# Optimization experiments

Measured on AMD Instinct MI355X. Metric: run time of the kernel, lower is better.

The kernel has to match this reference:

```python
import jax, jax.numpy as jnp
import numpy as np
from jax import lax

EPS = 1e-5

def _ln(x, g, b):
    m = x.mean(-1, keepdims=True)
    v = x.var(-1, keepdims=True)
    return (x - m) * lax.rsqrt(v + EPS) * g + b

def _conv(x, w, b=None, groups=1, pad=0):
    y = lax.conv_general_dilated(x, w, (1, 1), [(pad, pad), (pad, pad)],
                                 feature_group_count=groups,
                                 dimension_numbers=('NCHW', 'OIHW', 'NCHW'))
    return y if b is None else y + b[None, :, None, None]

def _pscan(A, X):
    # linear recurrence h_t = A_t * h_{t-1} + X_t via associative scan over axis 1
    def comb(c1, c2):
        a1, x1 = c1
        a2, x2 = c2
        return a1 * a2, a2 * x1 + x2
    return lax.associative_scan(comb, (A, X), axis=1)[1]

def setup_inputs():
    B, T, D, H, W, K, E = 2, 24, 32, 64, 64, 3, 2
    key = jax.random.key(0)
    ks = jax.random.split(key, 30)
    r = lambda i, shp, s=1.0: jax.random.normal(ks[i], shp, jnp.float32) * s
    return dict(
        x_re=r(0, (B, T, D, H, W)), x_im=r(1, (B, T, D, H, W)),
        h_re=r(2, (B * H * W, 1, D)), h_im=r(3, (B * H * W, 1, D)),
        flux_re=r(4, (B, D), 0.5), flux_im=r(5, (B, D), 0.5),
        dt_seq=jax.random.uniform(ks[6], (B, T), jnp.float32, 0.05, 0.15),
        ln_s_g=jnp.ones((2 * D,)), ln_s_b=jnp.zeros((2 * D,)),
        conv_w=r(7, (2 * D, 2 * D, K, K), 0.05), conv_b=jnp.zeros((2 * D,)),
        ln_t_g=jnp.ones((2 * D,)), ln_t_b=jnp.zeros((2 * D,)),
        W_re=jnp.eye(D, dtype=jnp.float32) + r(8, (D, D), 0.1), W_im=r(9, (D, D), 0.1),
        lam_flux=r(10, (D,), 0.5), bf_re=r(11, (D,), 0.5), bf_im=r(12, (D,), 0.5),
        c_re=r(13, (D,), 0.5), c_im=r(14, (D,), 0.5),
        g_w=r(15, (D,), 0.5), g_b=jnp.zeros((D,)),
        a_decay=r(16, (D,), 0.5), b_freq=r(17, (D,), 0.5),
        ffn_w1=r(18, (2 * D, 2 * D * E), 0.05), ffn_b1=jnp.zeros((2 * D * E,)),
        ffn_w2=r(19, (2 * D * E, 2 * D), 0.05), ffn_b2=jnp.zeros((2 * D,)),
        sg_w1=r(20, (D, 2 * D, 1, 1), 0.05), sg_b1=jnp.zeros((D,)),
        sg_dw=r(21, (D, 1, 3, 3), 0.05),
        sg_w2=r(22, (D, D, 1, 1), 0.05), sg_b2=jnp.zeros((D,)),
    )

def reference(x_re, x_im, h_re, h_im, flux_re, flux_im, dt_seq,
              ln_s_g, ln_s_b, conv_w, conv_b, ln_t_g, ln_t_b,
              W_re, W_im, lam_flux, bf_re, bf_im, c_re, c_im, g_w, g_b,
              a_decay, b_freq, ffn_w1, ffn_b1, ffn_w2, ffn_b2,
              sg_w1, sg_b1, sg_dw, sg_w2, sg_b2):
    x = x_re + 1j * x_im                                  # [B,T,D,H,W] complex64
    B, T, D, H, W = x.shape
    K = conv_w.shape[-1]
    # ---- spatial (Clifford-style) conv with residual ----
    xf = x.reshape(B * T, D, H, W)
    xr = jnp.concatenate([xf.real, xf.imag], axis=1)      # [BT,2D,H,W]
    xn = _ln(xr.transpose(0, 2, 3, 1), ln_s_g, ln_s_b).transpose(0, 3, 1, 2)
    xs = _conv(xn, conv_w, conv_b, pad=K // 2)
    xf = xf + (xs[:, :D] + 1j * xs[:, D:])
    x = xf.reshape(B, T, D, H, W)
    # ---- eigen-basis encode ----
    Wb = W_re + 1j * W_im
    Wb_inv = jnp.linalg.inv(Wb)
    x_eig = jnp.einsum('bthwd,de->bthwe', x.transpose(0, 1, 3, 4, 2), Wb)  # [B,T,H,W,D]
    x_mean = x_eig.mean(axis=(2, 3))                      # [B,T,D]
    # ---- global flux scan over time ----
    dt = dt_seq[:, :, None]                               # [B,T,1]
    A_flux = jnp.exp(-jax.nn.softplus(lam_flux) * dt).astype(x_eig.dtype)  # [B,T,D]
    X_flux = (bf_re + 1j * bf_im) * x_mean * dt
    flux_seq = _pscan(A_flux, X_flux)
    flux_seq = flux_seq + (flux_re + 1j * flux_im)[:, None, :] * jnp.cumprod(A_flux, axis=1)
    source_seq = flux_seq * (c_re + 1j * c_im)            # [B,T,D] complex
    gate_seq = jax.nn.sigmoid(flux_seq.real * g_w + g_b)  # [B,T,D] real
    flux_out = flux_seq[:, -1]
    # ---- spatial gate modulation, batched over B*T (no python loop over T) ----
    xc = jnp.concatenate([x_eig.real, x_eig.imag], axis=-1)        # [B,T,H,W,2D]
    sf = xc.reshape(B * T, H, W, 2 * D).transpose(0, 3, 1, 2)
    g = jax.nn.silu(_conv(sf, sg_w1, sg_b1))
    g = _conv(g, sg_dw, None, groups=D, pad=1)
    g = jax.nn.sigmoid(_conv(g, sg_w2, sg_b2))                     # [BT,D,H,W]
    sp_gate = g.transpose(0, 2, 3, 1).reshape(B, T, H, W, D)
    gate_comb = gate_seq[:, :, None, None, :] * sp_gate            # [B,T,H,W,D]
    src = source_seq[:, :, None, None, :]
    forcing = x_eig * gate_comb + src * (1.0 - gate_comb)
    # ---- transition operators (ZOH discretization) ----
    lam = -jax.nn.softplus(a_decay) + 1j * b_freq                  # [D]
    op_decay = jnp.exp(lam * dt)                                   # [B,T,D] complex
    op_forcing = (op_decay - 1.0) / lam
    u_t = forcing * op_forcing[:, :, None, None, :]
    h_prev = (h_re + 1j * h_im).reshape(B, H, W, D)
    u_t = u_t.at[:, 0].add(h_prev * op_decay[:, 0][:, None, None, :])
    # ---- per-pixel temporal pscan ----
    A_full = jnp.broadcast_to(op_decay[:, :, None, None, :], u_t.shape)
    u_out = _pscan(A_full, u_t)                                    # [B,T,H,W,D]
    h_out = u_out[:, -1].reshape(B * H * W, 1, D)
    # ---- decode + temporal LN/FFN residual ----
    dec = jnp.einsum('bthwe,ed->bthwd', u_out, Wb_inv).transpose(0, 1, 4, 2, 3)
    df = dec.reshape(B * T, D, H, W)
    dr = jnp.concatenate([df.real, df.imag], axis=1).transpose(0, 2, 3, 1)  # [BT,H,W,2D]
    dn = _ln(dr, ln_t_g, ln_t_b)
    hid = jax.nn.silu(dn @ ffn_w1 + ffn_b1)
    out2 = hid @ ffn_w2 + ffn_b2
    delta = (out2[..., :D] + 1j * out2[..., D:]).transpose(0, 3, 1, 2)
    xo = (df + delta).reshape(B, T, D, H, W)
    z = x + xo
    out_main = jnp.stack([z.real, z.imag], axis=0)
    out_h = jnp.stack([h_out.real, h_out.imag], axis=0)
    out_flux = jnp.stack([flux_out.real, flux_out.imag], axis=0)
    return out_main, out_h, out_flux
```

## Files before the change

kernel.cpp:

```cpp
#include <hip/hip_runtime.h>
#include <math.h>

#define BB 2
#define TT 24
#define DD 32
#define HWp 4096
#define NN (BB*TT)
#define PIX (NN*HWp)
#define C2 (2*DD)

#define MAIN_RE 0
#define MAIN_IM (NN*DD*HWp)
#define HOUT_RE (2*NN*DD*HWp)
#define HOUT_IM (HOUT_RE + BB*HWp*DD)
#define FLUX_RE (HOUT_RE + 2*BB*HWp*DD)
#define FLUX_IM (FLUX_RE + BB*DD)

#define WS_XN   0
#define WS_XU   (WS_XN + PIX*32)
#define WS_XE   (WS_XU + PIX*32)
#define WS_G1   (WS_XE + PIX*C2)
#define WS_G2   (WS_G1 + PIX*DD)
#define WS_WINV (WS_G2 + PIX*DD)
#define WS_SUMS (WS_WINV + 2048)
#define WS_GATE (WS_SUMS + 3072)
#define WS_SRCR (WS_GATE + 1536)
#define WS_SRCI (WS_SRCR + 1536)
#define WS_ODR  (WS_SRCI + 1536)
#define WS_ODI  (WS_ODR + 1536)
#define WS_OFR  (WS_ODI + 1536)
#define WS_OFI  (WS_OFR + 1536)
#define WS_WPK  (WS_OFI + 1536)
#define WS_PART (WS_WPK + 18432)
#define WS_WE   (WS_PART + 49152)
#define WS_SG   (WS_WE + 2048)
#define WS_WIB  (WS_SG + 1024)

typedef __attribute__((ext_vector_type(8))) short bf16x8;
typedef __attribute__((ext_vector_type(4))) float f32x4;
union FU { unsigned u[4]; bf16x8 f; };
union FU4 { uint4 v; unsigned u[4]; bf16x8 f; };

__device__ __forceinline__ float sigmoidf_(float x) { return 1.f / (1.f + expf(-x)); }
__device__ __forceinline__ float softplusf_(float x) { return log1pf(expf(x)); }
__device__ __forceinline__ unsigned short f2bf(float f) {
  unsigned u = __float_as_uint(f);
  return (unsigned short)((u + 0x7FFFu + ((u >> 16) & 1u)) >> 16);
}
__device__ __forceinline__ unsigned pk2(float lo, float hi) {
  return (unsigned)f2bf(lo) | ((unsigned)f2bf(hi) << 16);
}
__device__ __forceinline__ float bf2f(unsigned short u) {
  return __uint_as_float((unsigned)u << 16);
}

__global__ void __launch_bounds__(256) k_prep(
    const float* __restrict__ xre, const float* __restrict__ xim,
    const float* __restrict__ g, const float* __restrict__ b,
    const float* __restrict__ Wre, const float* __restrict__ Wim,
    const float* __restrict__ conv_w, const float* __restrict__ sgw1,
    float* __restrict__ ws) {
  int bid = blockIdx.x;
  int tid = threadIdx.x;

  if (bid < 768) {
    int gid = bid * 256 + tid;
    int n = gid >> 12, p = gid & 4095;
    float v[64];
    float s = 0.f;
#pragma unroll
    for (int c = 0; c < 32; ++c) { v[c] = xre[(n * 32 + c) * 4096 + p]; s += v[c]; }
#pragma unroll
    for (int c = 0; c < 32; ++c) { v[32 + c] = xim[(n * 32 + c) * 4096 + p]; s += v[32 + c]; }
    float m = s * (1.f / 64.f);
    float vs = 0.f;
#pragma unroll
    for (int c = 0; c < 64; ++c) { float d = v[c] - m; vs += d * d; }
    float rs = rsqrtf(vs * (1.f / 64.f) + 1e-5f);
#pragma unroll
    for (int c = 0; c < 64; ++c) v[c] = (v[c] - m) * rs * g[c] + b[c];
    uint4* dst = (uint4*)ws + gid * 8;
#pragma unroll
    for (int q = 0; q < 8; ++q) {
      uint4 u;
      u.x = pk2(v[q * 8 + 0], v[q * 8 + 1]);
      u.y = pk2(v[q * 8 + 2], v[q * 8 + 3]);
      u.z = pk2(v[q * 8 + 4], v[q * 8 + 5]);
      u.w = pk2(v[q * 8 + 6], v[q * 8 + 7]);
      dst[q] = u;
    }
    return;
  }

  if (bid <= 783) {
    int slice = bid - 768;
    unsigned short* wpk = (unsigned short*)(ws + WS_WPK);
#pragma unroll
    for (int i = 0; i < 9; ++i) {
      int idx = slice * 2304 + i * 256 + tid;
      int tap = idx >> 12;
      int rem = idx & 4095;
      int oc = rem >> 6, ci = rem & 63;
      wpk[idx] = f2bf(conv_w[(oc * 64 + ci) * 9 + tap]);
    }
    return;
  }

  {
    int t = (bid - 784) * 256 + tid;
    unsigned* we = (unsigned*)(ws + WS_WE);
    unsigned* sg = (unsigned*)(ws + WS_SG);
    {
      int oc = t >> 5, kp = t & 31;
      sg[t] = pk2(sgw1[oc * 64 + 2 * kp], sgw1[oc * 64 + 2 * kp + 1]);
    }
#pragma unroll
    for (int h2 = 0; h2 < 2; ++h2) {
      int idx = t + h2 * 1024;
      int j = idx >> 5, kp = idx & 31;
      float v[2];
#pragma unroll
      for (int h = 0; h < 2; ++h) {
        int k = 2 * kp + h;
        float x;
        if (j < 32) x = (k < 32) ? Wre[k * 32 + j] : -Wim[(k - 32) * 32 + j];
        else        x = (k < 32) ? Wim[k * 32 + (j - 32)] : Wre[(k - 32) * 32 + (j - 32)];
        v[h] = x;
      }
      we[idx] = pk2(v[0], v[1]);
    }
  }
}

__global__ void __launch_bounds__(256) k_conv(
    const unsigned* __restrict__ xnb_u, const unsigned short* __restrict__ wpk,
    const float* __restrict__ bconv,
    const float* __restrict__ xre, const float* __restrict__ xim,
    unsigned* __restrict__ xub,
    const float* __restrict__ Wre, const float* __restrict__ Wim,
    unsigned* __restrict__ wib) {
  __shared__ unsigned xls[8448];
  __shared__ int piv_s;
  __shared__ float prs[2];
  int bid = blockIdx.x;
  int tid = threadIdx.x;

  if (bid == 0) {
    float* Mre = (float*)xls;
    float* Mim = (float*)xls + 2048;
    float* fre = (float*)xls + 4096;
    float* fim = (float*)xls + 4128;
    for (int idx = tid; idx < 2048; idx += 256) {
      int i = idx >> 6, j = idx & 63;
      if (j < 32) { Mre[idx] = Wre[i * 32 + j]; Mim[idx] = Wim[i * 32 + j]; }
      else        { Mre[idx] = (j - 32 == i) ? 1.f : 0.f; Mim[idx] = 0.f; }
    }
    __syncthreads();
    for (int k = 0; k < 32; ++k) {
      if (tid < 32) {
        int r = tid;
        float re = Mre[r * 64 + k], im = Mim[r * 64 + k];
        float mm = (r >= k) ? (fabsf(re) + fabsf(im)) : -1.f;
        int best = r;
#pragma unroll
        for (int off = 16; off > 0; off >>= 1) {
          float m2 = __shfl_xor(mm, off);
          int b2 = __shfl_xor(best, off);
          if (m2 > mm || (m2 == mm && b2 < best)) { mm = m2; best = b2; }
        }
        float pvr = __shfl(re, best);
        float pvi = __shfl(im, best);
        if (tid == 0) {
          float dd = pvr * pvr + pvi * pvi;
          piv_s = best;
          prs[0] = pvr / dd;
          prs[1] = -pvi / dd;
        }
      }
      __syncthreads();
      int pv = piv_s;
      float pr = prs[0], pi = prs[1];
      if (tid < 64) {
        int l = tid;
        float kr = Mre[k * 64 + l], ki = Mim[k * 64 + l];
        float vr = Mre[pv * 64 + l], vi = Mim[pv * 64 + l];
        Mre[pv * 64 + l] = kr; Mim[pv * 64 + l] = ki;
        Mre[k * 64 + l] = vr * pr - vi * pi;
        Mim[k * 64 + l] = vr * pi + vi * pr;
        if (l == k) { fre[pv] = kr; fim[pv] = ki; }
        if (l < 32 && l != pv && l != k) {
          fre[l] = Mre[l * 64 + k];
          fim[l] = Mim[l * 64 + k];
        }
      }
      __syncthreads();
      for (int idx = tid; idx < 2048; idx += 256) {
        int i = idx >> 6, j = idx & 63;
        if (i != k) {
          float fr = fre[i], fi2 = fim[i];
          float ar = Mre[k * 64 + j], ai = Mim[k * 64 + j];
          Mre[idx] -= fr * ar - fi2 * ai;
          Mim[idx] -= fr * ai + fi2 * ar;
        }
      }
      __syncthreads();
    }
    for (int idx = tid; idx < 2048; idx += 256) {
      int j = idx >> 5, kp = idx & 31;
      float v[2];
#pragma unroll
      for (int h = 0; h < 2; ++h) {
        int kk = 2 * kp + h;
        float x;
        if (j < 32) x = (kk < 32) ? Mre[kk * 64 + 32 + j] : -Mim[(kk - 32) * 64 + 32 + j];
        else        x = (kk < 32) ? Mim[kk * 64 + 32 + (j - 32)] : Mre[(kk - 32) * 64 + 32 + (j - 32)];
        v[h] = x;
      }
      wib[idx] = pk2(v[0], v[1]);
    }
    return;
  }

  int cb = bid - 1;
  int n = cb >> 4;
  int y0 = (cb & 15) * 4;
  int wv = tid >> 6, l = tid & 63;
  int l15 = l & 15, l4 = l >> 4;

  const uint4* xnb4 = (const uint4*)xnb_u;

  f32x4 acc[4][4];
#pragma unroll
  for (int Nt = 0; Nt < 4; ++Nt) {
    float bb = bconv[Nt * 16 + l15];
#pragma unroll
    for (int mt = 0; mt < 4; ++mt) acc[mt][Nt] = (f32x4){bb, bb, bb, bb};
  }

  const uint4* wq = (const uint4*)wpk;
#pragma unroll
  for (int h = 0; h < 2; ++h) {
    if (h) __syncthreads();
    for (int idx = tid; idx < 396; idx += 256) {
      int r = idx / 66, c = idx - r * 66;
      int y = y0 - 1 + r, x = c - 1;
      bool valid = ((unsigned)y < 64u) & ((unsigned)x < 64u);
      int pg = n * 4096 + y * 64 + x;
      uint4 z; z.x = z.y = z.z = z.w = 0u;
#pragma unroll
      for (int q = 0; q < 4; ++q) {
        uint4 v = valid ? xnb4[pg * 8 + h * 4 + q] : z;
        *(uint4*)&xls[idx * 20 + q * 4] = v;
      }
    }
    __syncthreads();

#pragma unroll
    for (int tap = 0; tap < 9; ++tap) {
      int ky = tap / 3, kx = tap - ky * 3;
      int rowbase = (wv + ky) * 66 + kx + l15;
      FU4 B[4];
#pragma unroll
      for (int Nt = 0; Nt < 4; ++Nt)
        B[Nt].v = wq[tap * 512 + (Nt * 16 + l15) * 8 + h * 4 + l4];
#pragma unroll
      for (int mt = 0; mt < 4; ++mt) {
        FU4 A;
        A.v = *(const uint4*)&xls[(rowbase + mt * 16) * 20 + l4 * 4];
#pragma unroll
        for (int Nt = 0; Nt < 4; ++Nt)
          acc[mt][Nt] = __builtin_amdgcn_mfma_f32_16x16x32_bf16(A.f, B[Nt].f, acc[mt][Nt], 0, 0, 0);
      }
    }
  }
  __syncthreads();

  unsigned short (*xsb)[66] = (unsigned short(*)[66])xls;
#pragma unroll
  for (int Nt = 0; Nt < 4; ++Nt) {
    int oc = Nt * 16 + l15;
    int d = oc & 31;
    const float* resid = (oc < 32) ? xre : xim;
    const float* rsd = resid + (n * 32 + d) * 4096;
#pragma unroll
    for (int mt = 0; mt < 4; ++mt) {
      int lp0 = wv * 64 + mt * 16 + l4 * 4;
      int pixbase = y0 * 64 + lp0;
#pragma unroll
      for (int r = 0; r < 4; ++r)
        xsb[lp0 + r][oc] = f2bf(rsd[pixbase + r] + acc[mt][Nt][r]);
    }
  }
  __syncthreads();

  int pixG0 = n * 4096 + y0 * 64;
#pragma unroll
  for (int i = 0; i < 8; ++i) {
    int idx = tid + 256 * i;
    int lp = idx >> 3, q4 = idx & 7;
    uint4 v;
    v.x = xls[lp * 33 + q4 * 4 + 0];
    v.y = xls[lp * 33 + q4 * 4 + 1];
    v.z = xls[lp * 33 + q4 * 4 + 2];
    v.w = xls[lp * 33 + q4 * 4 + 3];
    ((uint4*)xub)[(pixG0 + lp) * 8 + q4] = v;
  }
}

__global__ void __launch_bounds__(256) k_xeig(
    const unsigned* __restrict__ xub, const unsigned* __restrict__ weP,
    const unsigned* __restrict__ sgP, unsigned short* __restrict__ xeb,
    unsigned short* __restrict__ g1b, const float* __restrict__ sgb1,
    float* __restrict__ part) {
  __shared__ unsigned WeT[64][35];
  __shared__ unsigned SgT[32][35];
  __shared__ unsigned xp[64][35];
  __shared__ float xef[64][67];

  int tid = threadIdx.x;
  int gbase = blockIdx.x * 256;
  int l = tid & 63, wv = tid >> 6;
  int l15 = l & 15, l4 = l >> 4;
  int p64 = l, q = wv;
  const uint4* xub4 = (const uint4*)xub;

  {
#pragma unroll
    for (int i = 0; i < 8; ++i) {
      int idx = tid + i * 256;
      WeT[idx >> 5][idx & 31] = weP[idx];
    }
#pragma unroll
    for (int i = 0; i < 4; ++i) {
      int idx = tid + i * 256;
      SgT[idx >> 5][idx & 31] = sgP[idx];
    }
  }
  float ssum[16];
#pragma unroll
  for (int i = 0; i < 16; ++i) ssum[i] = 0.f;
  __syncthreads();

  for (int ph = 0; ph < 4; ++ph) {
    int gg = gbase + ph * 64 + p64;
    int arow = wv * 16 + l15;
    int pixG = gbase + ph * 64 + arow;

    FU4 a0, a1;
    a0.v = xub4[pixG * 8 + l4];
    a1.v = xub4[pixG * 8 + 4 + l4];
#pragma unroll
    for (int Nt = 0; Nt < 4; ++Nt) {
      f32x4 acc = (f32x4){0.f, 0.f, 0.f, 0.f};
      FU b0f, b1f;
      int brow = Nt * 16 + l15;
#pragma unroll
      for (int jj = 0; jj < 4; ++jj) {
        b0f.u[jj] = WeT[brow][l4 * 4 + jj];
        b1f.u[jj] = WeT[brow][16 + l4 * 4 + jj];
      }
      acc = __builtin_amdgcn_mfma_f32_16x16x32_bf16(a0.f, b0f.f, acc, 0, 0, 0);
      acc = __builtin_amdgcn_mfma_f32_16x16x32_bf16(a1.f, b1f.f, acc, 0, 0, 0);
#pragma unroll
      for (int r = 0; r < 4; ++r)
        xef[wv * 16 + l4 * 4 + r][Nt * 16 + l15] = acc[r];
    }
    __syncthreads();

    float xo[16];
#pragma unroll
    for (int i = 0; i < 16; ++i) {
      xo[i] = xef[p64][q * 16 + i];
      ssum[i] += xo[i];
      xeb[(q * 16 + i) * PIX + gg] = f2bf(xo[i]);
    }
#pragma unroll
    for (int ii = 0; ii < 8; ++ii)
      xp[p64][q * 8 + ii] = pk2(xo[2 * ii], xo[2 * ii + 1]);
    __syncthreads();

    FU c0, c1;
#pragma unroll
    for (int jj = 0; jj < 4; ++jj) {
      c0.u[jj] = xp[arow][l4 * 4 + jj];
      c1.u[jj] = xp[arow][16 + l4 * 4 + jj];
    }
#pragma unroll
    for (int Nt = 0; Nt < 2; ++Nt) {
      float bb = sgb1[Nt * 16 + l15];
      f32x4 acc = (f32x4){bb, bb, bb, bb};
      FU b0f, b1f;
      int brow = Nt * 16 + l15;
#pragma unroll
      for (int jj = 0; jj < 4; ++jj) {
        b0f.u[jj] = SgT[brow][l4 * 4 + jj];
        b1f.u[jj] = SgT[brow][16 + l4 * 4 + jj];
      }
      acc = __builtin_amdgcn_mfma_f32_16x16x32_bf16(c0.f, b0f.f, acc, 0, 0, 0);
      acc = __builtin_amdgcn_mfma_f32_16x16x32_bf16(c1.f, b1f.f, acc, 0, 0, 0);
#pragma unroll
      for (int r = 0; r < 4; ++r) {
        float v = acc[r];
        xef[wv * 16 + l4 * 4 + r][Nt * 16 + l15] = v * sigmoidf_(v);
      }
    }
    __syncthreads();

#pragma unroll
    for (int i = 0; i < 8; ++i)
      g1b[(q * 8 + i) * PIX + gg] = f2bf(xef[p64][q * 8 + i]);
    __syncthreads();
  }

#pragma unroll
  for (int i = 0; i < 16; ++i) {
    float v = ssum[i];
    v += __shfl_xor(v, 1);
    v += __shfl_xor(v, 2);
    v += __shfl_xor(v, 4);
    v += __shfl_xor(v, 8);
    v += __shfl_xor(v, 16);
    v += __shfl_xor(v, 32);
    if (l == 0) part[blockIdx.x * 64 + q * 16 + i] = v;
  }
}

__global__ void k_flux(float* __restrict__ ws, float* __restrict__ out,
                       const float* __restrict__ dt_seq,
                       const float* __restrict__ flux_re, const float* __restrict__ flux_im,
                       const float* __restrict__ lam_flux,
                       const float* __restrict__ bf_re, const float* __restrict__ bf_im,
                       const float* __restrict__ c_re, const float* __restrict__ c_im,
                       const float* __restrict__ g_w, const float* __restrict__ g_b,
                       const float* __restrict__ a_decay, const float* __restrict__ b_freq) {
  int tid = threadIdx.x;
  if (tid >= 64) return;
  int b = tid >> 5, e = tid & 31;
  float sp_lf = softplusf_(lam_flux[e]);
  float lr = -softplusf_(a_decay[e]);
  float li = b_freq[e];
  float den = lr * lr + li * li;
  float bfr = bf_re[e], bfi = bf_im[e];
  float cr = c_re[e], ci = c_im[e];
  float fr = flux_re[b * 32 + e], fi = flux_im[b * 32 + e];
  const float* part = ws + WS_PART;
  for (int t = 0; t < 24; ++t) {
    int n = b * 24 + t;
    float dt = dt_seq[n];
    float A = expf(-sp_lf * dt);
    float xmr = 0.f, xmi = 0.f;
#pragma unroll
    for (int j = 0; j < 16; ++j) {
      xmr += part[(n * 16 + j) * 64 + e];
      xmi += part[(n * 16 + j) * 64 + 32 + e];
    }
    xmr *= (1.f / 4096.f);
    xmi *= (1.f / 4096.f);
    float Xr = (bfr * xmr - bfi * xmi) * dt;
    float Xi = (bfr * xmi + bfi * xmr) * dt;
    fr = A * fr + Xr;
    fi = A * fi + Xi;
    ws[WS_GATE + n * 32 + e] = sigmoidf_(fr * g_w[e] + g_b[e]);
    ws[WS_SRCR + n * 32 + e] = fr * cr - fi * ci;
    ws[WS_SRCI + n * 32 + e] = fr * ci + fi * cr;
    float er = expf(lr * dt);
    float odr = er * cosf(li * dt);
    float odi = er * sinf(li * dt);
    ws[WS_ODR + n * 32 + e] = odr;
    ws[WS_ODI + n * 32 + e] = odi;
    float nr = odr - 1.f, ni = odi;
    ws[WS_OFR + n * 32 + e] = (nr * lr + ni * li) / den;
    ws[WS_OFI + n * 32 + e] = (ni * lr - nr * li) / den;
  }
  out[FLUX_RE + b * 32 + e] = fr;
  out[FLUX_IM + b * 32 + e] = fi;
}

__global__ void __launch_bounds__(256) k_gate(
    const unsigned short* __restrict__ g1b, unsigned short* __restrict__ spgb,
    const float* __restrict__ dw, const float* __restrict__ w2,
    const float* __restrict__ b2) {
  __shared__ float g2s[128][33];
  int tid = threadIdx.x;
  int l = tid & 63;
  int wv = tid >> 6;
  int r = wv >> 1, h = wv & 1;
  int pixbase = blockIdx.x * 128;
  int n = pixbase >> 12;
  int y = ((pixbase & 4095) >> 6) + r;
  int g = pixbase + r * 64 + l;
  int rp = r * 64 + l;

#pragma unroll
  for (int c = 0; c < 16; ++c) {
    int oc = h * 16 + c;
    const unsigned short* src = g1b + oc * PIX + n * 4096;
    const float* w = dw + oc * 9;
    float r0 = (y > 0)  ? bf2f(src[(y - 1) * 64 + l]) : 0.f;
    float r1 = bf2f(src[y * 64 + l]);
    float r2 = (y < 63) ? bf2f(src[(y + 1) * 64 + l]) : 0.f;
    float l0 = __shfl_up(r0, 1), t0 = __shfl_down(r0, 1);
    float l1 = __shfl_up(r1, 1), t1 = __shfl_down(r1, 1);
    float l2 = __shfl_up(r2, 1), t2 = __shfl_down(r2, 1);
    if (l == 0)  { l0 = 0.f; l1 = 0.f; l2 = 0.f; }
    if (l == 63) { t0 = 0.f; t1 = 0.f; t2 = 0.f; }
    float acc = 0.f;
    acc = fmaf(l0, w[0], acc); acc = fmaf(r0, w[1], acc); acc = fmaf(t0, w[2], acc);
    acc = fmaf(l1, w[3], acc); acc = fmaf(r1, w[4], acc); acc = fmaf(t1, w[5], acc);
    acc = fmaf(l2, w[6], acc); acc = fmaf(r2, w[7], acc); acc = fmaf(t2, w[8], acc);
    g2s[rp][oc] = acc;
  }
  __syncthreads();
  float g2a[32];
#pragma unroll
  for (int c = 0; c < 32; ++c) g2a[c] = g2s[rp][c];

#pragma unroll
  for (int c = 0; c < 16; ++c) {
    int e = h * 16 + c;
    float acc = b2[e];
#pragma unroll
    for (int k = 0; k < 32; ++k)
      acc = fmaf(g2a[k], w2[e * 32 + k], acc);
    spgb[e * PIX + g] = f2bf(sigmoidf_(acc));
  }
}

__global__ void __launch_bounds__(256) k_scan(
    unsigned short* __restrict__ ub, const unsigned short* __restrict__ spgb,
    const float* __restrict__ gate, const float* __restrict__ srcr,
    const float* __restrict__ srci, const float* __restrict__ ofr_p,
    const float* __restrict__ ofi_p, const float* __restrict__ odr_p,
    const float* __restrict__ odi_p,
    const float* __restrict__ hre, const float* __restrict__ him,
    float* __restrict__ out) {
  int p = blockIdx.x * 256 + threadIdx.x;
  int e = blockIdx.y;
  int b = blockIdx.z;
  float ur = 0.f, ui = 0.f;
  for (int t = 0; t < 24; ++t) {
    int n = b * 24 + t;
    int ie = n * 32 + e;
    int idx  = e * PIX + n * 4096 + p;
    int idxi = (32 + e) * PIX + n * 4096 + p;
    float gc = gate[ie] * bf2f(spgb[idx]);
    float xr = bf2f(ub[idx]), xi = bf2f(ub[idxi]);
    float om = 1.f - gc;
    float fr2 = xr * gc + srcr[ie] * om;
    float fi2 = xi * gc + srci[ie] * om;
    float ofr = ofr_p[ie], ofi = ofi_p[ie];
    float utr = fr2 * ofr - fi2 * ofi;
    float uti = fr2 * ofi + fi2 * ofr;
    if (t == 0) {
      int hb = (b * 4096 + p) * 32 + e;
      float hr = hre[hb], hi = him[hb];
      float odr0 = odr_p[ie], odi0 = odi_p[ie];
      utr += hr * odr0 - hi * odi0;
      uti += hr * odi0 + hi * odr0;
    }
    float ar = odr_p[ie], ai = odi_p[ie];
    float nr = ar * ur - ai * ui + utr;
    float ni = ar * ui + ai * ur + uti;
    ur = nr; ui = ni;
    ub[idx] = f2bf(ur);
    ub[idxi] = f2bf(ui);
  }
  out[HOUT_RE + (b * 4096 + p) * 32 + e] = ur;
  out[HOUT_IM + (b * 4096 + p) * 32 + e] = ui;
}

__global__ void __launch_bounds__(256) k_final(
    const unsigned short* __restrict__ ub, const unsigned* __restrict__ xub,
    float* __restrict__ out, const unsigned* __restrict__ wibP,
    const float* __restrict__ lg, const float* __restrict__ lb,
    const float* __restrict__ w1, const float* __restrict__ b1,
    const float* __restrict__ w2, const float* __restrict__ b2) {
  __shared__ unsigned wiT[64][35];
  __shared__ unsigned w1T[128][35];
  __shared__ unsigned w2T[64][67];
  __shared__ unsigned dnp[64][35];
  __shared__ unsigned ho[64][67];
  __shared__ float ps1[64][5];
  __shared__ float ps2[64][5];

  int tid = threadIdx.x;
  int gbase = blockIdx.x * 256;
  int l = tid & 63, wv = tid >> 6;
  int l15 = l & 15, l4 = l >> 4;
  int p64 = l, q = wv;
  const uint4* xub4 = (const uint4*)xub;

  {
#pragma unroll
    for (int i = 0; i < 8; ++i) {
      int idx = tid + i * 256;
      wiT[idx >> 5][idx & 31] = wibP[idx];
    }
    int hid = tid & 127, half = tid >> 7;
#pragma unroll
    for (int i = 0; i < 16; ++i) {
      int cp = half * 16 + i;
      w1T[hid][cp] = pk2(w1[(2 * cp) * 128 + hid], w1[(2 * cp + 1) * 128 + hid]);
    }
#pragma unroll
    for (int i = 0; i < 16; ++i) {
      int hp = wv * 16 + i;
      w2T[l][hp] = pk2(w2[(2 * hp) * 64 + l], w2[(2 * hp + 1) * 64 + l]);
    }
  }
  float bb1v[8], bb2v[4];
#pragma unroll
  for (int Hn = 0; Hn < 8; ++Hn) bb1v[Hn] = b1[Hn * 16 + l15];
#pragma unroll
  for (int On = 0; On < 4; ++On) bb2v[On] = b2[On * 16 + l15];

  unsigned uvp[8];
  FU4 xa, xb;
  {
    int gg = gbase + p64;
#pragma unroll
    for (int ii = 0; ii < 8; ++ii) {
      int c0 = q * 16 + 2 * ii;
      unsigned lo = ub[c0 * PIX + gg];
      unsigned hi = ub[(c0 + 1) * PIX + gg];
      uvp[ii] = lo | (hi << 16);
    }
    xa.v = xub4[gg * 8 + q * 2];
    xb.v = xub4[gg * 8 + q * 2 + 1];
  }
  __syncthreads();

  for (int ph = 0; ph < 4; ++ph) {
    int gg = gbase + ph * 64 + p64;
    int arow = wv * 16 + l15;

#pragma unroll
    for (int ii = 0; ii < 8; ++ii)
      dnp[p64][q * 8 + ii] = uvp[ii];
    if (ph < 3) {
      int gg2 = gg + 64;
#pragma unroll
      for (int ii = 0; ii < 8; ++ii) {
        int c0 = q * 16 + 2 * ii;
        unsigned lo = ub[c0 * PIX + gg2];
        unsigned hi = ub[(c0 + 1) * PIX + gg2];
        uvp[ii] = lo | (hi << 16);
      }
    }
    __syncthreads();

    {
      FU a0, a1;
#pragma unroll
      for (int jj = 0; jj < 4; ++jj) {
        a0.u[jj] = dnp[arow][l4 * 4 + jj];
        a1.u[jj] = dnp[arow][16 + l4 * 4 + jj];
      }
      float (*decf)[67] = (float(*)[67])ho;
#pragma unroll
      for (int Nt = 0; Nt < 4; ++Nt) {
        f32x4 acc = (f32x4){0.f, 0.f, 0.f, 0.f};
        FU b0f, b1f;
        int brow = Nt * 16 + l15;
#pragma unroll
        for (int jj = 0; jj < 4; ++jj) {
          b0f.u[jj] = wiT[brow][l4 * 4 + jj];
          b1f.u[jj] = wiT[brow][16 + l4 * 4 + jj];
        }
        acc = __builtin_amdgcn_mfma_f32_16x16x32_bf16(a0.f, b0f.f, acc, 0, 0, 0);
        acc = __builtin_amdgcn_mfma_f32_16x16x32_bf16(a1.f, b1f.f, acc, 0, 0, 0);
#pragma unroll
        for (int r = 0; r < 4; ++r)
          decf[wv * 16 + l4 * 4 + r][Nt * 16 + l15] = acc[r];
      }
    }
    __syncthreads();

    float dv[16];
    float s1 = 0.f, s2 = 0.f;
    {
      float (*decf)[67] = (float(*)[67])ho;
#pragma unroll
      for (int i = 0; i < 16; ++i) {
        dv[i] = decf[p64][q * 16 + i];
        s1 += dv[i];
        s2 += dv[i] * dv[i];
      }
    }
    ps1[p64][q] = s1;
    ps2[p64][q] = s2;
    __syncthreads();
    float m  = (ps1[p64][0] + ps1[p64][1] + ps1[p64][2] + ps1[p64][3]) * (1.f / 64.f);
    float e2 = (ps2[p64][0] + ps2[p64][1] + ps2[p64][2] + ps2[p64][3]) * (1.f / 64.f);
    float rs = rsqrtf(e2 - m * m + 1e-5f);
#pragma unroll
    for (int ii = 0; ii < 8; ++ii) {
      int c0 = q * 16 + 2 * ii;
      float a = (dv[2 * ii]     - m) * rs * lg[c0]     + lb[c0];
      float bvl = (dv[2 * ii + 1] - m) * rs * lg[c0 + 1] + lb[c0 + 1];
      dnp[p64][q * 8 + ii] = pk2(a, bvl);
    }
    __syncthreads();

    FU a0, a1;
#pragma unroll
    for (int jj = 0; jj < 4; ++jj) {
      a0.u[jj] = dnp[arow][l4 * 4 + jj];
      a1.u[jj] = dnp[arow][16 + l4 * 4 + jj];
    }
    f32x4 acc[8];
#pragma unroll
    for (int Hn = 0; Hn < 8; ++Hn) {
      float bb = bb1v[Hn];
      acc[Hn] = (f32x4){bb, bb, bb, bb};
      FU b0f, b1f;
      int brow = Hn * 16 + l15;
#pragma unroll
      for (int jj = 0; jj < 4; ++jj) {
        b0f.u[jj] = w1T[brow][l4 * 4 + jj];
        b1f.u[jj] = w1T[brow][16 + l4 * 4 + jj];
      }
      acc[Hn] = __builtin_amdgcn_mfma_f32_16x16x32_bf16(a0.f, b0f.f, acc[Hn], 0, 0, 0);
      acc[Hn] = __builtin_amdgcn_mfma_f32_16x16x32_bf16(a1.f, b1f.f, acc[Hn], 0, 0, 0);
    }
    unsigned short (*hidb)[134] = (unsigned short(*)[134])ho;
#pragma unroll
    for (int Hn = 0; Hn < 8; ++Hn) {
#pragma unroll
      for (int r = 0; r < 4; ++r) {
        float v = acc[Hn][r];
        v = v * sigmoidf_(v);
        hidb[wv * 16 + l4 * 4 + r][Hn * 16 + l15] = f2bf(v);
      }
    }
    __syncthreads();

    FU a2[4];
#pragma unroll
    for (int kk = 0; kk < 4; ++kk)
#pragma unroll
      for (int jj = 0; jj < 4; ++jj)
        a2[kk].u[jj] = ((unsigned(*)[67])ho)[arow][kk * 16 + l4 * 4 + jj];
    f32x4 acc2[4];
#pragma unroll
    for (int On = 0; On < 4; ++On) {
      float bb = bb2v[On];
      acc2[On] = (f32x4){bb, bb, bb, bb};
#pragma unroll
      for (int kk = 0; kk < 4; ++kk) {
        FU b2f;
#pragma unroll
        for (int jj = 0; jj < 4; ++jj)
          b2f.u[jj] = w2T[On * 16 + l15][kk * 16 + l4 * 4 + jj];
        acc2[On] = __builtin_amdgcn_mfma_f32_16x16x32_bf16(a2[kk].f, b2f.f, acc2[On], 0, 0, 0);
      }
    }
    float (*o2f)[67] = (float(*)[67])ho;
#pragma unroll
    for (int On = 0; On < 4; ++On)
#pragma unroll
      for (int r = 0; r < 4; ++r)
        o2f[wv * 16 + l4 * 4 + r][On * 16 + l15] = acc2[On][r];
    __syncthreads();

    {
      int nn = gg >> 12, pim = gg & 4095;
#pragma unroll
      for (int ii = 0; ii < 8; ++ii) {
        unsigned w = (ii < 4) ? xa.u[ii] : xb.u[ii - 4];
        float x0 = __uint_as_float(w << 16);
        float x1 = __uint_as_float(w & 0xFFFF0000u);
        int c0 = q * 16 + 2 * ii;
#pragma unroll
        for (int h = 0; h < 2; ++h) {
          int c = c0 + h;
          float xv = (h == 0) ? x0 : x1;
          float val = xv + o2f[p64][c] + dv[2 * ii + h];
          int d = c & 31;
          long off = ((c < 32) ? (long)MAIN_RE : (long)MAIN_IM) + (long)(nn * 32 + d) * 4096 + pim;
          out[off] = val;
        }
      }
      if (ph < 3) {
        int gg2 = gg + 64;
        xa.v = xub4[gg2 * 8 + q * 2];
        xb.v = xub4[gg2 * 8 + q * 2 + 1];
      }
    }
    __syncthreads();
  }
}

extern "C" void kernel_launch(void* const* d_in, const int* in_sizes, int n_in,
                              void* d_out, int out_size, void* d_ws, size_t ws_size,
                              hipStream_t stream) {
  (void)in_sizes; (void)n_in; (void)out_size; (void)ws_size;
  const float* xre      = (const float*)d_in[0];
  const float* xim      = (const float*)d_in[1];
  const float* hre      = (const float*)d_in[2];
  const float* him      = (const float*)d_in[3];
  const float* flux_re  = (const float*)d_in[4];
  const float* flux_im  = (const float*)d_in[5];
  const float* dt_seq   = (const float*)d_in[6];
  const float* ln_s_g   = (const float*)d_in[7];
  const float* ln_s_b   = (const float*)d_in[8];
  const float* conv_w   = (const float*)d_in[9];
  const float* conv_b   = (const float*)d_in[10];
  const float* ln_t_g   = (const float*)d_in[11];
  const float* ln_t_b   = (const float*)d_in[12];
  const float* W_re     = (const float*)d_in[13];
  const float* W_im     = (const float*)d_in[14];
  const float* lam_flux = (const float*)d_in[15];
  const float* bf_re    = (const float*)d_in[16];
  const float* bf_im    = (const float*)d_in[17];
  const float* c_re     = (const float*)d_in[18];
  const float* c_im     = (const float*)d_in[19];
  const float* g_w      = (const float*)d_in[20];
  const float* g_b      = (const float*)d_in[21];
  const float* a_decay  = (const float*)d_in[22];
  const float* b_freq   = (const float*)d_in[23];
  const float* ffn_w1   = (const float*)d_in[24];
  const float* ffn_b1   = (const float*)d_in[25];
  const float* ffn_w2   = (const float*)d_in[26];
  const float* ffn_b2   = (const float*)d_in[27];
  const float* sg_w1    = (const float*)d_in[28];
  const float* sg_b1    = (const float*)d_in[29];
  const float* sg_dw    = (const float*)d_in[30];
  const float* sg_w2    = (const float*)d_in[31];
  const float* sg_b2    = (const float*)d_in[32];
  float* out = (float*)d_out;
  float* ws  = (float*)d_ws;

  unsigned* xub = (unsigned*)(ws + WS_XU);
  unsigned short* xeb = (unsigned short*)(ws + WS_XE);
  unsigned short* g1b = (unsigned short*)(ws + WS_G1);
  unsigned short* spgb = (unsigned short*)(ws + WS_G2);

  k_prep<<<788, 256, 0, stream>>>(xre, xim, ln_s_g, ln_s_b, W_re, W_im,
                                  conv_w, sg_w1, ws);
  k_conv<<<769, 256, 0, stream>>>((const unsigned*)(ws + WS_XN),
                                  (const unsigned short*)(ws + WS_WPK),
                                  conv_b, xre, xim, xub,
                                  W_re, W_im, (unsigned*)(ws + WS_WIB));
  k_xeig<<<768, 256, 0, stream>>>(xub, (const unsigned*)(ws + WS_WE),
                                  (const unsigned*)(ws + WS_SG),
                                  xeb, g1b, sg_b1, ws + WS_PART);
  k_flux<<<1, 64, 0, stream>>>(ws, out, dt_seq, flux_re, flux_im, lam_flux,
                               bf_re, bf_im, c_re, c_im, g_w, g_b, a_decay, b_freq);
  k_gate<<<PIX / 128, 256, 0, stream>>>(g1b, spgb, sg_dw, sg_w2, sg_b2);
  k_scan<<<dim3(4096 / 256, 32, 2), 256, 0, stream>>>(xeb, spgb,
                                                      ws + WS_GATE, ws + WS_SRCR, ws + WS_SRCI,
                                                      ws + WS_OFR, ws + WS_OFI,
                                                      ws + WS_ODR, ws + WS_ODI,
                                                      hre, him, out);
  k_final<<<768, 256, 0, stream>>>(xeb, xub, out, (const unsigned*)(ws + WS_WIB),
                                   ln_t_g, ln_t_b, ffn_w1, ffn_b1, ffn_w2, ffn_b2);
}
```

Baseline: 242.2 us.

## Stage packed bf16 residual in prep and prefetch conv second channel half

Result: slower. 258.2 us (+6.6%).

```diff
diff --git a/kernel.cpp b/kernel.cpp
--- a/kernel.cpp
+++ b/kernel.cpp
@@ -19,6 +19,7 @@
 #define WS_XN   0
 #define WS_XU   (WS_XN + PIX*32)
 #define WS_XE   (WS_XU + PIX*32)
+#define WS_XR   (WS_XE + PIX*32)
 #define WS_G1   (WS_XE + PIX*C2)
 #define WS_G2   (WS_G1 + PIX*DD)
 #define WS_WINV (WS_G2 + PIX*DD)
@@ -53,6 +54,11 @@
 __device__ __forceinline__ float bf2f(unsigned short u) {
   return __uint_as_float((unsigned)u << 16);
 }
+__device__ __forceinline__ unsigned addbf2(unsigned a, unsigned b) {
+  float lo = __uint_as_float(a << 16) + __uint_as_float(b << 16);
+  float hi = __uint_as_float(a & 0xFFFF0000u) + __uint_as_float(b & 0xFFFF0000u);
+  return pk2(lo, hi);
+}
 
 __global__ void __launch_bounds__(256) k_prep(
     const float* __restrict__ xre, const float* __restrict__ xim,
@@ -72,6 +78,16 @@
     for (int c = 0; c < 32; ++c) { v[c] = xre[(n * 32 + c) * 4096 + p]; s += v[c]; }
 #pragma unroll
     for (int c = 0; c < 32; ++c) { v[32 + c] = xim[(n * 32 + c) * 4096 + p]; s += v[32 + c]; }
+    uint4* dstr = (uint4*)(ws + WS_XR) + gid * 8;
+#pragma unroll
+    for (int q = 0; q < 8; ++q) {
+      uint4 u;
+      u.x = pk2(v[q * 8 + 0], v[q * 8 + 1]);
+      u.y = pk2(v[q * 8 + 2], v[q * 8 + 3]);
+      u.z = pk2(v[q * 8 + 4], v[q * 8 + 5]);
+      u.w = pk2(v[q * 8 + 6], v[q * 8 + 7]);
+      dstr[q] = u;
+    }
     float m = s * (1.f / 64.f);
     float vs = 0.f;
 #pragma unroll
@@ -134,8 +150,7 @@
 
 __global__ void __launch_bounds__(256) k_conv(
     const unsigned* __restrict__ xnb_u, const unsigned short* __restrict__ wpk,
-    const float* __restrict__ bconv,
-    const float* __restrict__ xre, const float* __restrict__ xim,
+    const float* __restrict__ bconv, const unsigned* __restrict__ xrb,
     unsigned* __restrict__ xub,
     const float* __restrict__ Wre, const float* __restrict__ Wim,
     unsigned* __restrict__ wib) {
@@ -237,11 +252,11 @@
     for (int mt = 0; mt < 4; ++mt) acc[mt][Nt] = (f32x4){bb, bb, bb, bb};
   }
 
-  const uint4* wq = (const uint4*)wpk;
-#pragma unroll
-  for (int h = 0; h < 2; ++h) {
-    if (h) __syncthreads();
-    for (int idx = tid; idx < 396; idx += 256) {
+  uint4 pf[2][4];
+#pragma unroll
+  for (int it = 0; it < 2; ++it) {
+    int idx = tid + it * 256;
+    if (idx < 396) {
       int r = idx / 66, c = idx - r * 66;
       int y = y0 - 1 + r, x = c - 1;
       bool valid = ((unsigned)y < 64u) & ((unsigned)x < 64u);
@@ -249,12 +264,30 @@
       uint4 z; z.x = z.y = z.z = z.w = 0u;
 #pragma unroll
       for (int q = 0; q < 4; ++q) {
-        uint4 v = valid ? xnb4[pg * 8 + h * 4 + q] : z;
-        *(uint4*)&xls[idx * 20 + q * 4] = v;
-      }
-    }
-    __syncthreads();
-
+        uint4 v0 = valid ? xnb4[pg * 8 + q] : z;
+        *(uint4*)&xls[idx * 20 + q * 4] = v0;
+        pf[it][q] = valid ? xnb4[pg * 8 + 4 + q] : z;
+      }
+    }
+  }
+  __syncthreads();
+
+  const uint4* wq = (const uint4*)wpk;
+#pragma unroll
+  for (int h = 0; h < 2; ++h) {
+    if (h == 1) {
+      __syncthreads();
+#pragma unroll
+      for (int it = 0; it < 2; ++it) {
+        int idx = tid + it * 256;
+        if (idx < 396) {
+#pragma unroll
+          for (int q = 0; q < 4; ++q)
+            *(uint4*)&xls[idx * 20 + q * 4] = pf[it][q];
+        }
+      }
+      __syncthreads();
+    }
 #pragma unroll
     for (int tap = 0; tap < 9; ++tap) {
       int ky = tap / 3, kx = tap - ky * 3;
@@ -279,31 +312,34 @@
 #pragma unroll
   for (int Nt = 0; Nt < 4; ++Nt) {
     int oc = Nt * 16 + l15;
-    int d = oc & 31;
-    const float* resid = (oc < 32) ? xre : xim;
-    const float* rsd = resid + (n * 32 + d) * 4096;
 #pragma unroll
     for (int mt = 0; mt < 4; ++mt) {
       int lp0 = wv * 64 + mt * 16 + l4 * 4;
-      int pixbase = y0 * 64 + lp0;
 #pragma unroll
       for (int r = 0; r < 4; ++r)
-        xsb[lp0 + r][oc] = f2bf(rsd[pixbase + r] + acc[mt][Nt][r]);
+        xsb[lp0 + r][oc] = f2bf(acc[mt][Nt][r]);
     }
   }
   __syncthreads();
 
+  const uint4* xrb4 = (const uint4*)xrb;
   int pixG0 = n * 4096 + y0 * 64;
 #pragma unroll
   for (int i = 0; i < 8; ++i) {
     int idx = tid + 256 * i;
     int lp = idx >> 3, q4 = idx & 7;
-    uint4 v;
-    v.x = xls[lp * 33 + q4 * 4 + 0];
-    v.y = xls[lp * 33 + q4 * 4 + 1];
-    v.z = xls[lp * 33 + q4 * 4 + 2];
-    v.w = xls[lp * 33 + q4 * 4 + 3];
-    ((uint4*)xub)[(pixG0 + lp) * 8 + q4] = v;
+    uint4 cv;
+    cv.x = xls[lp * 33 + q4 * 4 + 0];
+    cv.y = xls[lp * 33 + q4 * 4 + 1];
+    cv.z = xls[lp * 33 + q4 * 4 + 2];
+    cv.w = xls[lp * 33 + q4 * 4 + 3];
+    uint4 rv = xrb4[(pixG0 + lp) * 8 + q4];
+    uint4 o;
+    o.x = addbf2(cv.x, rv.x);
+    o.y = addbf2(cv.y, rv.y);
+    o.z = addbf2(cv.z, rv.z);
+    o.w = addbf2(cv.w, rv.w);
+    ((uint4*)xub)[(pixG0 + lp) * 8 + q4] = o;
   }
 }
 
@@ -832,6 +868,7 @@
   float* ws  = (float*)d_ws;
 
   unsigned* xub = (unsigned*)(ws + WS_XU);
+  unsigned* xrb = (unsigned*)(ws + WS_XR);
   unsigned short* xeb = (unsigned short*)(ws + WS_XE);
   unsigned short* g1b = (unsigned short*)(ws + WS_G1);
   unsigned short* spgb = (unsigned short*)(ws + WS_G2);
@@ -840,7 +877,7 @@
                                   conv_w, sg_w1, ws);
   k_conv<<<769, 256, 0, stream>>>((const unsigned*)(ws + WS_XN),
                                   (const unsigned short*)(ws + WS_WPK),
-                                  conv_b, xre, xim, xub,
+                                  conv_b, (const unsigned*)xrb, xub,
                                   W_re, W_im, (unsigned*)(ws + WS_WIB));
   k_xeig<<<768, 256, 0, stream>>>(xub, (const unsigned*)(ws + WS_WE),
                                   (const unsigned*)(ws + WS_SG),
```
